# Kernel tuning notes

Measured on AMD Instinct MI355X. Metric: run time of the kernel, lower is better.

## Reference

```python
import jax, jax.numpy as jnp
import numpy as np

HIDDEN = 768
ENT = 9
D = 64  # inner_dim
BIG = 1e12


def _rope_tables(seq_len, dim):
    # layout after torch stack([sin,cos],-1).reshape: [sin0,cos0,sin1,cos1,...]
    pos = jnp.arange(seq_len, dtype=jnp.float32)[:, None]          # [S,1]
    inv = jnp.power(10000.0, -2.0 * jnp.arange(dim // 2, dtype=jnp.float32) / dim)
    ang = pos * inv                                                 # [S,D/2]
    # repeat_interleave(2): [c0,c0,c1,c1,...]
    cos = jnp.repeat(jnp.cos(ang), 2, axis=-1)[:, None, :]          # [S,1,D]
    sin = jnp.repeat(jnp.sin(ang), 2, axis=-1)[:, None, :]
    return sin, cos


def _rotate_half_interleaved(x):
    # stack([-x_odd, x_even], -1).reshape -> [-x1, x0, -x3, x2, ...]
    return jnp.stack([-x[..., 1::2], x[..., ::2]], axis=-1).reshape(x.shape)


def _multilabel_ce(logits, labels):
    # standard GlobalPointer multilabel categorical crossentropy
    B = logits.shape[0]
    y_pred = logits.reshape(B * ENT, -1)
    y_true = labels.reshape(B * ENT, -1)
    y_pred = (1.0 - 2.0 * y_true) * y_pred
    y_neg = y_pred - y_true * BIG
    y_pos = y_pred - (1.0 - y_true) * BIG
    neg = jnp.logaddexp(0.0, jax.scipy.special.logsumexp(y_neg, axis=-1))
    pos = jnp.logaddexp(0.0, jax.scipy.special.logsumexp(y_pos, axis=-1))
    return jnp.mean(neg + pos)


def setup_inputs() -> dict:
    key = jax.random.key(0)
    k1, k2, k3, k4 = jax.random.split(key, 4)
    B, S = 16, 512
    last_hidden_state = jax.random.normal(k1, (B, S, HIDDEN), dtype=jnp.float32)
    attention_mask = jnp.ones((B, S), dtype=jnp.int32)
    batch_labels = jax.random.randint(k2, (B, ENT, S, S), 0, 2).astype(jnp.int32)
    W = jax.random.normal(k3, (HIDDEN, ENT * D * 2), dtype=jnp.float32) * 0.02
    b = jnp.zeros((ENT * D * 2,), dtype=jnp.float32)
    return {"last_hidden_state": last_hidden_state, "attention_mask": attention_mask,
            "batch_labels": batch_labels, "W": W, "b": b}


def reference(last_hidden_state, attention_mask, batch_labels, W, b):
    B, S, _ = last_hidden_state.shape
    out = last_hidden_state @ W + b                     # [B,S,ENT*2D]
    out = out.reshape(B, S, ENT, 2 * D)
    qw, kw = out[..., :D], out[..., D:]                 # [B,S,ENT,D]

    sin, cos = _rope_tables(S, D)                       # [S,1,D]
    qw = qw * cos + _rotate_half_interleaved(qw) * sin
    kw = kw * cos + _rotate_half_interleaved(kw) * sin

    logits = jnp.einsum('bmhd,bnhd->bhmn', qw, kw)      # [B,ENT,S,S]

    pad = attention_mask.astype(jnp.float32)[:, None, None, :]  # mask over key dim n
    logits = logits * pad - (1.0 - pad) * BIG
    tril = jnp.tril(jnp.ones((S, S), dtype=jnp.float32), -1)
    logits = logits - tril * BIG
    temp_logits = logits / (D ** 0.5)

    loss = _multilabel_ce(temp_logits, batch_labels.astype(jnp.float32))
    return loss, temp_logits
```

## Files before the change

kernel.cpp:

```cpp
#include <hip/hip_runtime.h>
#include <hip/hip_bf16.h>

#define HID 768
#define ENTS 9
#define DD 64
#define NOUT 1152
#define BATCH 16
#define SEQ 512
#define BIGF 1000000000000.0f
#define BIG8 125000000000.0f
#define NCHUNK 16

typedef __attribute__((ext_vector_type(8))) short short8;
typedef __attribute__((ext_vector_type(4))) short short4_t;
typedef __attribute__((ext_vector_type(4))) float floatx4;
typedef __attribute__((ext_vector_type(2))) float floatx2;
typedef __attribute__((ext_vector_type(4))) int intx4;
typedef unsigned short ushort_t;

static __device__ __forceinline__ ushort_t f2bf(float x) {
    unsigned int u = __float_as_uint(x);
    unsigned int r = (u + 0x7FFFu + ((u >> 16) & 1u)) >> 16;
    return (ushort_t)r;
}

static __device__ __forceinline__ void gload16(const void* g, void* l) {
    __builtin_amdgcn_global_load_lds(
        (const __attribute__((address_space(1))) void*)g,
        (__attribute__((address_space(3))) void*)l, 16, 0, 0);
}

__global__ __launch_bounds__(256) void prep_kernel(
    const float* __restrict__ X, const float* __restrict__ W,
    float* __restrict__ sin_t, float* __restrict__ cos_t,
    ushort_t* __restrict__ Xb, ushort_t* __restrict__ Wt)
{
    const int tid = blockIdx.x * 256 + threadIdx.x;
    const int nth = gridDim.x * 256;

    for (int idx = tid; idx < SEQ * 32; idx += nth) {
        int m = idx >> 5, i = idx & 31;
        float inv = powf(10000.0f, -2.0f * (float)i / 64.0f);
        float ang = (float)m * inv;
        sin_t[idx] = sinf(ang);
        cos_t[idx] = cosf(ang);
    }
    for (int idx = tid; idx < NOUT * HID; idx += nth) {
        int n = idx / HID, k = idx - n * HID;
        Wt[idx] = f2bf(W[(size_t)k * NOUT + n]);
    }
    const int nx4 = BATCH * SEQ * HID / 4;
    for (int idx = tid; idx < nx4; idx += nth) {
        float4 f = *(const float4*)&X[idx * 4];
        ushort_t* p = &Xb[idx * 4];
        p[0] = f2bf(f.x); p[1] = f2bf(f.y); p[2] = f2bf(f.z); p[3] = f2bf(f.w);
    }
}

__global__ __launch_bounds__(256) void proj_rope_kernel(
    const ushort_t* __restrict__ Xb, const ushort_t* __restrict__ Wt,
    const float* __restrict__ bias,
    const float* __restrict__ sin_t, const float* __restrict__ cos_t,
    ushort_t* __restrict__ qbuf, ushort_t* __restrict__ kbuf)
{
    __shared__ ushort_t As[64 * 32];
    __shared__ ushort_t Bs[128 * 32];
    const int tid  = threadIdx.x;
    const int lane = tid & 63;
    const int wave = tid >> 6;
    const int bm = blockIdx.x * 64;
    const int bn = blockIdx.y * 128;
    const int wn = wave * 32;

    floatx4 acc[2][4];
    #pragma unroll
    for (int j = 0; j < 2; ++j)
        #pragma unroll
        for (int i = 0; i < 4; ++i) { floatx4 z = {0.f,0.f,0.f,0.f}; acc[j][i] = z; }

    const int rA = tid >> 2, qA = (tid & 3) * 8;
    const int rB1 = 64 + (tid >> 2);
    ushort_t* ldsA  = As + wave * 512;
    ushort_t* ldsB0 = Bs + wave * 512;
    ushort_t* ldsB1 = Bs + 2048 + wave * 512;

    const int g  = lane >> 4;
    const int lr = lane & 15;
    const int ko = g * 8;

    for (int kt = 0; kt < HID; kt += 32) {
        gload16(&Xb[(size_t)(bm + rA) * HID + kt + qA], ldsA);
        gload16(&Wt[(size_t)(bn + rA) * HID + kt + qA], ldsB0);
        gload16(&Wt[(size_t)(bn + rB1) * HID + kt + qA], ldsB1);
        __syncthreads();

        short8 a[4], b[2];
        #pragma unroll
        for (int i = 0; i < 4; ++i) a[i] = *(const short8*)&As[(i*16 + lr) * 32 + ko];
        #pragma unroll
        for (int j = 0; j < 2; ++j) b[j] = *(const short8*)&Bs[(wn + j*16 + lr) * 32 + ko];
        #pragma unroll
        for (int j = 0; j < 2; ++j)
            #pragma unroll
            for (int i = 0; i < 4; ++i)
                acc[j][i] = __builtin_amdgcn_mfma_f32_16x16x32_bf16(b[j], a[i], acc[j][i], 0, 0, 0);
        __syncthreads();
    }

    const int e = blockIdx.y;
    #pragma unroll
    for (int j = 0; j < 2; ++j) {
        const int n0  = bn + wn + j*16 + (g << 2);
        const int dd0 = n0 & 127;
        const bool isq = dd0 < DD;
        const int d0  = isq ? dd0 : dd0 - DD;
        const float4 bv = *(const float4*)&bias[n0];
        #pragma unroll
        for (int i = 0; i < 4; ++i) {
            const int m = bm + i*16 + lr;
            const int s  = m & (SEQ - 1);
            const int bb = m >> 9;
            const float c0f = cos_t[s*32 + (d0 >> 1)];
            const float s0f = sin_t[s*32 + (d0 >> 1)];
            const float c1f = cos_t[s*32 + (d0 >> 1) + 1];
            const float s1f = sin_t[s*32 + (d0 >> 1) + 1];
            const float v0 = acc[j][i][0] + bv.x;
            const float v1 = acc[j][i][1] + bv.y;
            const float v2 = acc[j][i][2] + bv.z;
            const float v3 = acc[j][i][3] + bv.w;
            const float o0 = v0 * c0f - v1 * s0f;
            const float o1 = v1 * c0f + v0 * s0f;
            const float o2 = v2 * c1f - v3 * s1f;
            const float o3 = v3 * c1f + v2 * s1f;
            short4_t sv = { (short)f2bf(o0), (short)f2bf(o1), (short)f2bf(o2), (short)f2bf(o3) };
            size_t oidx = (((size_t)(bb * ENTS + e) * SEQ) + s) * DD + d0;
            *(short4_t*)&(isq ? qbuf : kbuf)[oidx] = sv;
        }
    }
}

__global__ __launch_bounds__(256) void qk_mask_ce_kernel(
    const ushort_t* __restrict__ qbuf, const ushort_t* __restrict__ kbuf,
    const int* __restrict__ amask, const int* __restrict__ labels,
    float* __restrict__ logits, float* __restrict__ partials)
{
    __shared__ ushort_t Qs[128][72];
    __shared__ ushort_t Ks[128][72];
    __shared__ float ssn[4], ssp[4];
    const int tid  = threadIdx.x;

    const int wrk = (blockIdx.x & 7) * 288 + (blockIdx.x >> 3);
    const int bh = wrk >> 4;
    const int xy = wrk & 15;
    const int bx = xy >> 2, by = xy & 3;
    const int bm = bx * 128;
    const int bn = by * 128;
    const int b  = bh / ENTS;
    const int bhbase = bh << 18;

    if (bx > by) {
        const int c4 = (tid & 31) << 2;
        const int rr = tid >> 5;

        const intx4 pf = *(const intx4*)&amask[(b << 9) + bn + c4];
        floatx4 cv;
        #pragma unroll
        for (int e = 0; e < 4; ++e) cv[e] = (float)pf[e] * BIG8 - 2.0f * BIG8;
        float cvm1 = 0.f;
        if (c4 > 0) {
            const int pfm1 = amask[(b << 9) + bn + c4 - 1];
            cvm1 = (float)pfm1 * BIG8 - 2.0f * BIG8;
        }
        const floatx4 sh = { cvm1, cv.x, cv.y, cv.z };
        const floatx2 h2 = { cv.y, cv.z };

        int cnt = 0;
        for (int pass = 0; pass < 16; ++pass) {
            const int m = bm + pass * 8 + rr;
            const int off = bhbase + (m << 9) + bn + c4;
            const intx4 y4 = *(const intx4*)&labels[off];
            #pragma unroll
            for (int e = 0; e < 4; ++e) cnt += (y4[e] & 1) & pf[e];
            if (c4 == 0) {
                logits[off] = cv.x;
                *(floatx2*)&logits[off + 1] = h2;
            } else {
                *(floatx4*)&logits[off - 1] = sh;
            }
            if (c4 == 124) logits[off + 3] = cv.w;
        }

        #pragma unroll
        for (int o = 32; o > 0; o >>= 1) cnt += __shfl_down(cnt, o);
        if ((tid & 63) == 0) ssn[tid >> 6] = (float)cnt;
        __syncthreads();
        if (tid == 0) {
            float SP = ssn[0] + ssn[1] + ssn[2] + ssn[3];
            floatx2 res = { 0.f, SP };
            *(floatx2*)&partials[(size_t)(bh * NCHUNK + xy) * 2] = res;
        }
        return;
    }

    const int lane = tid & 63;
    const int wave = tid >> 6;
    const int wm = (wave >> 1) * 64;
    const int wn = (wave & 1) * 64;
    const size_t base = (size_t)bh * SEQ * DD;

    const int g  = lane >> 4;
    const int lr = lane & 15;
    const int ko = g * 8;
    const int r0 = bm + wm + lr;
    const int W  = bn + wn;
    const int n00 = W + (g << 2);

    const bool diag = (bx == by);

    intx4 yc[2][4];
    #pragma unroll
    for (int jh = 0; jh < 2; ++jh)
        #pragma unroll
        for (int i = 0; i < 4; ++i)
            yc[jh][i] = *(const intx4*)&labels[bhbase + ((r0 + i*16) << 9) + n00 + jh*16];

    floatx4 pm8[4], pc[4];
    #pragma unroll
    for (int j = 0; j < 4; ++j) {
        const intx4 p4 = *(const intx4*)&amask[(b << 9) + n00 + j*16];
        #pragma unroll
        for (int rg = 0; rg < 4; ++rg) {
            const float pf = (float)p4[rg];
            pm8[j][rg] = pf * 0.125f;
            pc[j][rg]  = (pf - 1.0f) * BIG8;
        }
    }

    {
        const int r  = tid >> 1;
        const int ks = (tid & 1) * 32;
        const ushort_t* gq = &qbuf[base + (size_t)(bm + r) * DD + ks];
        const ushort_t* gk = &kbuf[base + (size_t)(bn + r) * DD + ks];
        #pragma unroll
        for (int uu = 0; uu < 4; ++uu) {
            *(short8*)&Qs[r][ks + uu*8] = *(const short8*)(gq + uu*8);
            *(short8*)&Ks[r][ks + uu*8] = *(const short8*)(gk + uu*8);
        }
    }
    __syncthreads();

    short8 a[2][4];
    #pragma unroll
    for (int kk = 0; kk < 2; ++kk)
        #pragma unroll
        for (int i = 0; i < 4; ++i)
            a[kk][i] = *(const short8*)&Qs[wm + i*16 + lr][kk*32 + ko];

    float smn = 0.f, smp = 0.f;
    float tl[4];
    float* __restrict__ lgb = logits + bhbase;

    #pragma unroll
    for (int jp = 0; jp < 2; ++jp) {
        const int jA = jp * 2, jB = jp * 2 + 1;

        floatx4 accA[4], accB[4];
        #pragma unroll
        for (int i = 0; i < 4; ++i) { floatx4 z = {0.f,0.f,0.f,0.f}; accA[i] = z; accB[i] = z; }
        #pragma unroll
        for (int kk = 0; kk < 2; ++kk) {
            const short8 bfA = *(const short8*)&Ks[wn + jA*16 + lr][kk*32 + ko];
            const short8 bfB = *(const short8*)&Ks[wn + jB*16 + lr][kk*32 + ko];
            #pragma unroll
            for (int i = 0; i < 4; ++i) {
                accA[i] = __builtin_amdgcn_mfma_f32_16x16x32_bf16(bfA, a[kk][i], accA[i], 0, 0, 0);
                accB[i] = __builtin_amdgcn_mfma_f32_16x16x32_bf16(bfB, a[kk][i], accB[i], 0, 0, 0);
            }
        }

        unsigned int yb = 0;
        {
            int cnt = 0;
            #pragma unroll
            for (int jh = 0; jh < 2; ++jh)
                #pragma unroll
                for (int i = 0; i < 4; ++i)
                    #pragma unroll
                    for (int rg = 0; rg < 4; ++rg) {
                        yb |= (unsigned)(yc[jh][i][rg] & 1) << cnt;
                        ++cnt;
                    }
        }

        if (jp == 0) {
            #pragma unroll
            for (int jh = 0; jh < 2; ++jh)
                #pragma unroll
                for (int i = 0; i < 4; ++i)
                    yc[jh][i] = *(const intx4*)&labels[bhbase + ((r0 + i*16) << 9) + n00 + (2 + jh)*16];
        }

        int cnt = 0;
        #pragma unroll
        for (int half = 0; half < 2; ++half) {
            const int j = half ? jB : jA;
            const floatx4 pm = pm8[j], pcj = pc[j];
            const int n0j = W + j*16 + (g << 2);
            #pragma unroll
            for (int i = 0; i < 4; ++i) {
                const int m = r0 + i*16;
                const int d = m - n0j;
                floatx4 v = half ? accB[i] : accA[i];
                #pragma unroll
                for (int rg = 0; rg < 4; ++rg) {
                    float t = fmaf(v[rg], pm[rg], pcj[rg]);
                    if (diag && (d > rg)) t -= BIG8;
                    v[rg] = t;
                    const int yy = (int)((yb >> cnt) & 1u);
                    const float uu = __uint_as_float(__float_as_uint(t) ^ ((unsigned)yy << 31));
                    const float arg = yy ? (uu - BIG8) : uu;
                    const float e = __expf(arg);
                    const float ep = yy ? e : 0.0f;
                    smp += ep;
                    smn += e - ep;
                    ++cnt;
                }
                if (half) accB[i] = v; else accA[i] = v;
            }
        }

        #pragma unroll
        for (int i = 0; i < 4; ++i) {
            const floatx4 vA = accA[i], vB = accB[i];
            const int m = r0 + i*16;
            float* __restrict__ row = lgb + (m << 9);
            const float sameA  = __shfl(vA.w, (lane - 16) & 63);
            const float tailA  = __shfl(tl[i], lr + 48);
            const float sameB  = __shfl(vB.w, (lane - 16) & 63);
            const float crossB = __shfl(vA.w, lr + 48);
            const float uA0 = (g == 0) ? tailA  : sameA;
            const float uB0 = (g == 0) ? crossB : sameB;
            if (jp == 0 && g == 0) {
                row[W] = vA.x;
                floatx2 h2 = { vA.y, vA.z };
                *(floatx2*)&row[W + 1] = h2;
            } else {
                floatx4 uA = { uA0, vA.x, vA.y, vA.z };
                *(floatx4*)&row[W + jA*16 + (g << 2) - 1] = uA;
            }
            floatx4 uB = { uB0, vB.x, vB.y, vB.z };
            *(floatx4*)&row[W + jB*16 + (g << 2) - 1] = uB;
            tl[i] = vB.w;
        }
    }

    if (g == 3) {
        #pragma unroll
        for (int i = 0; i < 4; ++i) {
            const int m = r0 + i*16;
            lgb[(m << 9) + W + 63] = tl[i];
        }
    }

    #pragma unroll
    for (int off = 32; off > 0; off >>= 1) {
        smn += __shfl_down(smn, off);
        smp += __shfl_down(smp, off);
    }
    if (lane == 0) { ssn[wave] = smn; ssp[wave] = smp; }
    __syncthreads();
    if (tid == 0) {
        float SN = ssn[0] + ssn[1] + ssn[2] + ssn[3];
        float SP = ssp[0] + ssp[1] + ssp[2] + ssp[3];
        floatx2 res = { SN, SP };
        *(floatx2*)&partials[(size_t)(bh * NCHUNK + xy) * 2] = res;
    }
}

static __device__ __forceinline__ float lae0(float x) {
    return fmaxf(x, 0.f) + log1pf(__expf(-fabsf(x)));
}

__global__ __launch_bounds__(256) void ce_final_kernel(
    const float* __restrict__ partials, float* __restrict__ out)
{
    __shared__ float red[256];
    const int t = threadIdx.x;
    float val = 0.f;
    if (t < BATCH * ENTS) {
        float SN = 0.f, SP = 0.f;
        for (int c = 0; c < NCHUNK; ++c) {
            SN += partials[(size_t)(t * NCHUNK + c) * 2];
            SP += partials[(size_t)(t * NCHUNK + c) * 2 + 1];
        }
        const float neg = log1pf(SN);
        const float pos = lae0(BIG8 + logf(SP));
        val = neg + pos;
    }
    red[t] = val;
    __syncthreads();
    for (int s2 = 128; s2 > 0; s2 >>= 1) {
        if (t < s2) red[t] += red[t + s2];
        __syncthreads();
    }
    if (t == 0) out[0] = red[0] / (float)(BATCH * ENTS);
}

extern "C" void kernel_launch(void* const* d_in, const int* in_sizes, int n_in,
                              void* d_out, int out_size, void* d_ws, size_t ws_size,
                              hipStream_t stream) {
    const float* X      = (const float*)d_in[0];
    const int*   amask  = (const int*)d_in[1];
    const int*   labels = (const int*)d_in[2];
    const float* W      = (const float*)d_in[3];
    const float* bias   = (const float*)d_in[4];

    float* out    = (float*)d_out;
    float* logits = out + 1;

    float* sin_t = (float*)d_ws;
    float* cos_t = sin_t + SEQ * 32;
    ushort_t* Xb   = (ushort_t*)(cos_t + SEQ * 32);
    ushort_t* Wt   = Xb + (size_t)BATCH * SEQ * HID;
    ushort_t* qbuf = Wt + (size_t)NOUT * HID;
    ushort_t* kbuf = qbuf + (size_t)BATCH * ENTS * SEQ * DD;
    float* partials = (float*)(kbuf + (size_t)BATCH * ENTS * SEQ * DD);

    prep_kernel<<<1024, 256, 0, stream>>>(X, W, sin_t, cos_t, Xb, Wt);
    proj_rope_kernel<<<dim3(128, 9), 256, 0, stream>>>(Xb, Wt, bias, sin_t, cos_t, qbuf, kbuf);
    qk_mask_ce_kernel<<<2304, 256, 0, stream>>>(qbuf, kbuf, amask, labels, logits, partials);
    ce_final_kernel<<<1, 256, 0, stream>>>(partials, out);
}
```

Before: 129.8 us.

## Process whole row strip per block, reusing Q registers across column tiles

The QK/mask/CE kernel now gives each block one 128-row strip of a (batch, entity) pair. Q fragments are loaded once from global straight into registers, and the block loops over the upper-triangular column tiles, reloading only K into shared memory for each tile. Fully masked lower tiles keep their own blocks, and the grid shrinks from 2304 to 1440 blocks. This removes redundant Q loads and the Q shared-memory buffer. In exchange, blocks get uneven amounts of work (one to four tiles), the K reloads are serialized with extra barriers, and fewer blocks are available to hide latency.

```diff
diff --git a/kernel.cpp b/kernel.cpp
--- a/kernel.cpp
+++ b/kernel.cpp
@@ -144,21 +144,23 @@
     const int* __restrict__ amask, const int* __restrict__ labels,
     float* __restrict__ logits, float* __restrict__ partials)
 {
-    __shared__ ushort_t Qs[128][72];
     __shared__ ushort_t Ks[128][72];
     __shared__ float ssn[4], ssp[4];
     const int tid  = threadIdx.x;
 
-    const int wrk = (blockIdx.x & 7) * 288 + (blockIdx.x >> 3);
-    const int bh = wrk >> 4;
-    const int xy = wrk & 15;
-    const int bx = xy >> 2, by = xy & 3;
-    const int bm = bx * 128;
-    const int bn = by * 128;
+    const int wrk = (blockIdx.x & 7) * 180 + (blockIdx.x >> 3);
+    const int bh = wrk / 10;
+    const int t  = wrk - bh * 10;
     const int b  = bh / ENTS;
     const int bhbase = bh << 18;
 
-    if (bx > by) {
+    if (t >= 4) {
+        const int u = t - 4;
+        int bx, by;
+        if (u < 3)      { by = 0; bx = u + 1; }
+        else if (u < 5) { by = 1; bx = u - 1; }
+        else            { bx = 3; by = 2; }
+        const int bm = bx * 128, bn = by * 128;
         const int c4 = (tid & 31) << 2;
         const int rr = tid >> 5;
 
@@ -197,11 +199,13 @@
         if (tid == 0) {
             float SP = ssn[0] + ssn[1] + ssn[2] + ssn[3];
             floatx2 res = { 0.f, SP };
-            *(floatx2*)&partials[(size_t)(bh * NCHUNK + xy) * 2] = res;
+            *(floatx2*)&partials[(size_t)(bh * NCHUNK + bx * 4 + by) * 2] = res;
         }
         return;
     }
 
+    const int bx = t;
+    const int bm = bx * 128;
     const int lane = tid & 63;
     const int wave = tid >> 6;
     const int wm = (wave >> 1) * 64;
@@ -212,168 +216,173 @@
     const int lr = lane & 15;
     const int ko = g * 8;
     const int r0 = bm + wm + lr;
-    const int W  = bn + wn;
-    const int n00 = W + (g << 2);
-
-    const bool diag = (bx == by);
+    const int gc = wn + (g << 2);
+
+    short8 a[2][4];
+    #pragma unroll
+    for (int kk = 0; kk < 2; ++kk)
+        #pragma unroll
+        for (int i = 0; i < 4; ++i)
+            a[kk][i] = *(const short8*)&qbuf[base + (size_t)(r0 + i*16) * DD + kk*32 + ko];
 
     intx4 yc[2][4];
     #pragma unroll
     for (int jh = 0; jh < 2; ++jh)
         #pragma unroll
         for (int i = 0; i < 4; ++i)
-            yc[jh][i] = *(const intx4*)&labels[bhbase + ((r0 + i*16) << 9) + n00 + jh*16];
-
-    floatx4 pm8[4], pc[4];
-    #pragma unroll
-    for (int j = 0; j < 4; ++j) {
-        const intx4 p4 = *(const intx4*)&amask[(b << 9) + n00 + j*16];
-        #pragma unroll
-        for (int rg = 0; rg < 4; ++rg) {
-            const float pf = (float)p4[rg];
-            pm8[j][rg] = pf * 0.125f;
-            pc[j][rg]  = (pf - 1.0f) * BIG8;
-        }
-    }
-
+            yc[jh][i] = *(const intx4*)&labels[bhbase + ((r0 + i*16) << 9) + bx*128 + gc + jh*16];
+
+    const int rS  = tid >> 1;
+    const int ksS = (tid & 1) * 32;
     {
-        const int r  = tid >> 1;
-        const int ks = (tid & 1) * 32;
-        const ushort_t* gq = &qbuf[base + (size_t)(bm + r) * DD + ks];
-        const ushort_t* gk = &kbuf[base + (size_t)(bn + r) * DD + ks];
-        #pragma unroll
-        for (int uu = 0; uu < 4; ++uu) {
-            *(short8*)&Qs[r][ks + uu*8] = *(const short8*)(gq + uu*8);
-            *(short8*)&Ks[r][ks + uu*8] = *(const short8*)(gk + uu*8);
-        }
+        const ushort_t* gk = &kbuf[base + (size_t)(bx*128 + rS) * DD + ksS];
+        #pragma unroll
+        for (int uu = 0; uu < 4; ++uu)
+            *(short8*)&Ks[rS][ksS + uu*8] = *(const short8*)(gk + uu*8);
     }
     __syncthreads();
 
-    short8 a[2][4];
-    #pragma unroll
-    for (int kk = 0; kk < 2; ++kk)
-        #pragma unroll
-        for (int i = 0; i < 4; ++i)
-            a[kk][i] = *(const short8*)&Qs[wm + i*16 + lr][kk*32 + ko];
-
-    float smn = 0.f, smp = 0.f;
-    float tl[4];
     float* __restrict__ lgb = logits + bhbase;
 
-    #pragma unroll
-    for (int jp = 0; jp < 2; ++jp) {
-        const int jA = jp * 2, jB = jp * 2 + 1;
-
-        floatx4 accA[4], accB[4];
-        #pragma unroll
-        for (int i = 0; i < 4; ++i) { floatx4 z = {0.f,0.f,0.f,0.f}; accA[i] = z; accB[i] = z; }
-        #pragma unroll
-        for (int kk = 0; kk < 2; ++kk) {
-            const short8 bfA = *(const short8*)&Ks[wn + jA*16 + lr][kk*32 + ko];
-            const short8 bfB = *(const short8*)&Ks[wn + jB*16 + lr][kk*32 + ko];
-            #pragma unroll
-            for (int i = 0; i < 4; ++i) {
-                accA[i] = __builtin_amdgcn_mfma_f32_16x16x32_bf16(bfA, a[kk][i], accA[i], 0, 0, 0);
-                accB[i] = __builtin_amdgcn_mfma_f32_16x16x32_bf16(bfB, a[kk][i], accB[i], 0, 0, 0);
-            }
-        }
-
-        unsigned int yb = 0;
-        {
-            int cnt = 0;
-            #pragma unroll
-            for (int jh = 0; jh < 2; ++jh)
+    for (int by = bx; by < 4; ++by) {
+        const int W    = by*128 + wn;
+        const bool diag = (by == bx);
+        float smn = 0.f, smp = 0.f;
+        float tl[4];
+
+        #pragma unroll
+        for (int jp = 0; jp < 2; ++jp) {
+            const int jA = jp * 2, jB = jp * 2 + 1;
+
+            floatx4 accA[4], accB[4];
+            #pragma unroll
+            for (int i = 0; i < 4; ++i) { floatx4 z = {0.f,0.f,0.f,0.f}; accA[i] = z; accB[i] = z; }
+            #pragma unroll
+            for (int kk = 0; kk < 2; ++kk) {
+                const short8 bfA = *(const short8*)&Ks[wn + jA*16 + lr][kk*32 + ko];
+                const short8 bfB = *(const short8*)&Ks[wn + jB*16 + lr][kk*32 + ko];
                 #pragma unroll
-                for (int i = 0; i < 4; ++i)
+                for (int i = 0; i < 4; ++i) {
+                    accA[i] = __builtin_amdgcn_mfma_f32_16x16x32_bf16(bfA, a[kk][i], accA[i], 0, 0, 0);
+                    accB[i] = __builtin_amdgcn_mfma_f32_16x16x32_bf16(bfB, a[kk][i], accB[i], 0, 0, 0);
+                }
+            }
+
+            unsigned int yb = 0;
+            {
+                int cc = 0;
+                #pragma unroll
+                for (int jh = 0; jh < 2; ++jh)
+                    #pragma unroll
+                    for (int i = 0; i < 4; ++i)
+                        #pragma unroll
+                        for (int rg = 0; rg < 4; ++rg) {
+                            yb |= (unsigned)(yc[jh][i][rg] & 1) << cc;
+                            ++cc;
+                        }
+            }
+
+            if (jp == 0) {
+                #pragma unroll
+                for (int jh = 0; jh < 2; ++jh)
+                    #pragma unroll
+                    for (int i = 0; i < 4; ++i)
+                        yc[jh][i] = *(const intx4*)&labels[bhbase + ((r0 + i*16) << 9) + by*128 + gc + (2 + jh)*16];
+            } else if (by < 3) {
+                #pragma unroll
+                for (int jh = 0; jh < 2; ++jh)
+                    #pragma unroll
+                    for (int i = 0; i < 4; ++i)
+                        yc[jh][i] = *(const intx4*)&labels[bhbase + ((r0 + i*16) << 9) + (by+1)*128 + gc + jh*16];
+            }
+
+            const intx4 p4A = *(const intx4*)&amask[(b << 9) + by*128 + gc + jA*16];
+            const intx4 p4B = *(const intx4*)&amask[(b << 9) + by*128 + gc + jB*16];
+
+            int cc = 0;
+            #pragma unroll
+            for (int half = 0; half < 2; ++half) {
+                const int j = half ? jB : jA;
+                const intx4 p4 = half ? p4B : p4A;
+                const int n0j = W + j*16 + (g << 2);
+                #pragma unroll
+                for (int i = 0; i < 4; ++i) {
+                    const int m = r0 + i*16;
+                    const int d = m - n0j;
+                    floatx4 v = half ? accB[i] : accA[i];
                     #pragma unroll
                     for (int rg = 0; rg < 4; ++rg) {
-                        yb |= (unsigned)(yc[jh][i][rg] & 1) << cnt;
-                        ++cnt;
+                        const float pf = (float)p4[rg];
+                        float tt = fmaf(v[rg], pf * 0.125f, (pf - 1.0f) * BIG8);
+                        if (diag && (d > rg)) tt -= BIG8;
+                        v[rg] = tt;
+                        const int yy = (int)((yb >> cc) & 1u);
+                        const float uu = __uint_as_float(__float_as_uint(tt) ^ ((unsigned)yy << 31));
+                        const float arg = yy ? (uu - BIG8) : uu;
+                        const float e = __expf(arg);
+                        const float ep = yy ? e : 0.0f;
+                        smp += ep;
+                        smn += e - ep;
+                        ++cc;
                     }
-        }
-
-        if (jp == 0) {
-            #pragma unroll
-            for (int jh = 0; jh < 2; ++jh)
-                #pragma unroll
-                for (int i = 0; i < 4; ++i)
-                    yc[jh][i] = *(const intx4*)&labels[bhbase + ((r0 + i*16) << 9) + n00 + (2 + jh)*16];
-        }
-
-        int cnt = 0;
-        #pragma unroll
-        for (int half = 0; half < 2; ++half) {
-            const int j = half ? jB : jA;
-            const floatx4 pm = pm8[j], pcj = pc[j];
-            const int n0j = W + j*16 + (g << 2);
+                    if (half) accB[i] = v; else accA[i] = v;
+                }
+            }
+
+            #pragma unroll
+            for (int i = 0; i < 4; ++i) {
+                const floatx4 vA = accA[i], vB = accB[i];
+                const int m = r0 + i*16;
+                float* __restrict__ row = lgb + (m << 9);
+                const float sameA  = __shfl(vA.w, (lane - 16) & 63);
+                const float tailA  = __shfl(tl[i], lr + 48);
+                const float sameB  = __shfl(vB.w, (lane - 16) & 63);
+                const float crossB = __shfl(vA.w, lr + 48);
+                const float uA0 = (g == 0) ? tailA  : sameA;
+                const float uB0 = (g == 0) ? crossB : sameB;
+                if (jp == 0 && g == 0) {
+                    row[W] = vA.x;
+                    floatx2 h2 = { vA.y, vA.z };
+                    *(floatx2*)&row[W + 1] = h2;
+                } else {
+                    floatx4 uA = { uA0, vA.x, vA.y, vA.z };
+                    *(floatx4*)&row[W + jA*16 + (g << 2) - 1] = uA;
+                }
+                floatx4 uB = { uB0, vB.x, vB.y, vB.z };
+                *(floatx4*)&row[W + jB*16 + (g << 2) - 1] = uB;
+                tl[i] = vB.w;
+            }
+        }
+
+        if (g == 3) {
             #pragma unroll
             for (int i = 0; i < 4; ++i) {
                 const int m = r0 + i*16;
-                const int d = m - n0j;
-                floatx4 v = half ? accB[i] : accA[i];
-                #pragma unroll
-                for (int rg = 0; rg < 4; ++rg) {
-                    float t = fmaf(v[rg], pm[rg], pcj[rg]);
-                    if (diag && (d > rg)) t -= BIG8;
-                    v[rg] = t;
-                    const int yy = (int)((yb >> cnt) & 1u);
-                    const float uu = __uint_as_float(__float_as_uint(t) ^ ((unsigned)yy << 31));
-                    const float arg = yy ? (uu - BIG8) : uu;
-                    const float e = __expf(arg);
-                    const float ep = yy ? e : 0.0f;
-                    smp += ep;
-                    smn += e - ep;
-                    ++cnt;
-                }
-                if (half) accB[i] = v; else accA[i] = v;
-            }
-        }
-
-        #pragma unroll
-        for (int i = 0; i < 4; ++i) {
-            const floatx4 vA = accA[i], vB = accB[i];
-            const int m = r0 + i*16;
-            float* __restrict__ row = lgb + (m << 9);
-            const float sameA  = __shfl(vA.w, (lane - 16) & 63);
-            const float tailA  = __shfl(tl[i], lr + 48);
-            const float sameB  = __shfl(vB.w, (lane - 16) & 63);
-            const float crossB = __shfl(vA.w, lr + 48);
-            const float uA0 = (g == 0) ? tailA  : sameA;
-            const float uB0 = (g == 0) ? crossB : sameB;
-            if (jp == 0 && g == 0) {
-                row[W] = vA.x;
-                floatx2 h2 = { vA.y, vA.z };
-                *(floatx2*)&row[W + 1] = h2;
-            } else {
-                floatx4 uA = { uA0, vA.x, vA.y, vA.z };
-                *(floatx4*)&row[W + jA*16 + (g << 2) - 1] = uA;
-            }
-            floatx4 uB = { uB0, vB.x, vB.y, vB.z };
-            *(floatx4*)&row[W + jB*16 + (g << 2) - 1] = uB;
-            tl[i] = vB.w;
-        }
-    }
-
-    if (g == 3) {
-        #pragma unroll
-        for (int i = 0; i < 4; ++i) {
-            const int m = r0 + i*16;
-            lgb[(m << 9) + W + 63] = tl[i];
-        }
-    }
-
-    #pragma unroll
-    for (int off = 32; off > 0; off >>= 1) {
-        smn += __shfl_down(smn, off);
-        smp += __shfl_down(smp, off);
-    }
-    if (lane == 0) { ssn[wave] = smn; ssp[wave] = smp; }
-    __syncthreads();
-    if (tid == 0) {
-        float SN = ssn[0] + ssn[1] + ssn[2] + ssn[3];
-        float SP = ssp[0] + ssp[1] + ssp[2] + ssp[3];
-        floatx2 res = { SN, SP };
-        *(floatx2*)&partials[(size_t)(bh * NCHUNK + xy) * 2] = res;
+                lgb[(m << 9) + W + 63] = tl[i];
+            }
+        }
+
+        #pragma unroll
+        for (int off = 32; off > 0; off >>= 1) {
+            smn += __shfl_down(smn, off);
+            smp += __shfl_down(smp, off);
+        }
+        if (lane == 0) { ssn[wave] = smn; ssp[wave] = smp; }
+        __syncthreads();
+        if (tid == 0) {
+            float SN = ssn[0] + ssn[1] + ssn[2] + ssn[3];
+            float SP = ssp[0] + ssp[1] + ssp[2] + ssp[3];
+            floatx2 res = { SN, SP };
+            *(floatx2*)&partials[(size_t)(bh * NCHUNK + bx * 4 + by) * 2] = res;
+        }
+
+        if (by < 3) {
+            const ushort_t* gk = &kbuf[base + (size_t)((by+1)*128 + rS) * DD + ksS];
+            #pragma unroll
+            for (int uu = 0; uu < 4; ++uu)
+                *(short8*)&Ks[rS][ksS + uu*8] = *(const short8*)(gk + uu*8);
+            __syncthreads();
+        }
     }
 }
 
@@ -428,6 +437,6 @@
 
     prep_kernel<<<1024, 256, 0, stream>>>(X, W, sin_t, cos_t, Xb, Wt);
     proj_rope_kernel<<<dim3(128, 9), 256, 0, stream>>>(Xb, Wt, bias, sin_t, cos_t, qbuf, kbuf);
-    qk_mask_ce_kernel<<<2304, 256, 0, stream>>>(qbuf, kbuf, amask, labels, logits, partials);
+    qk_mask_ce_kernel<<<1440, 256, 0, stream>>>(qbuf, kbuf, amask, labels, logits, partials);
     ce_final_kernel<<<1, 256, 0, stream>>>(partials, out);
 }
```

After: 157.2 us. 1.21x slower.
